# Performance work log

Hardware: AMD Instinct MI355X
Metric: run time of the kernel (lower is better)

Reference implementation:

```python
import jax, jax.numpy as jnp
import numpy as np

B, L, D_MODEL = 2, 4096, 512
HEADS = 8
DH = D_MODEL // HEADS
M = 266  # round(DH * ln(DH)) = round(64 * 4.1589)


def setup_inputs() -> dict:
    key = jax.random.key(0)
    ks = jax.random.split(key, 12)
    s = 0.02
    d = D_MODEL
    return {
        "query": jax.random.normal(ks[0], (B, L, d), jnp.float32),
        "key": jax.random.normal(ks[1], (B, L, d), jnp.float32),
        "value": jax.random.normal(ks[2], (B, L, d), jnp.float32),
        "Wq": jax.random.normal(ks[3], (d, d), jnp.float32) * s,
        "bq": jnp.zeros((d,), jnp.float32),
        "Wk": jax.random.normal(ks[4], (d, d), jnp.float32) * s,
        "bk": jnp.zeros((d,), jnp.float32),
        "Wv": jax.random.normal(ks[5], (d, d), jnp.float32) * s,
        "bv": jnp.zeros((d,), jnp.float32),
        "Wout": jax.random.normal(ks[6], (d, d), jnp.float32) * s,
        "bout": jnp.zeros((d,), jnp.float32),
        "random_features": jax.random.normal(ks[7], (M, DH), jnp.float32),
    }


def reference(query, key, value, Wq, bq, Wk, bk, Wv, bv, Wout, bout, random_features):
    bs, sl, dm = query.shape
    H, Dh = HEADS, dm // HEADS

    def lin(x, W, b):
        return x @ W.T + b

    def to_heads(x):  # [B,L,dm] -> [L,B,H,Dh]  (matches torch [L,B,H,*] layout)
        return x.reshape(bs, sl, H, Dh).transpose(1, 0, 2, 3)

    q = to_heads(lin(query, Wq, bq))
    k = to_heads(lin(key, Wk, bk))
    v = to_heads(lin(value, Wv, bv))

    scale = dm ** 0.25
    q = q / scale
    k = k / scale

    # project onto random features: W_t is random_features^T, [Dh,M]
    pq = jnp.einsum('lbhd,md->lbhm', q, random_features)
    pk = jnp.einsum('lbhd,md->lbhm', k, random_features)
    # exp kernel: exp(h + x) with h = -||x||^2 / 2
    hq = -0.5 * jnp.sum(q * q, axis=-1, keepdims=True)
    hk = -0.5 * jnp.sum(k * k, axis=-1, keepdims=True)
    q_prime = jnp.exp(hq + pq)  # [L,B,H,M]
    k_prime = jnp.exp(hk + pk)  # [L,B,H,M]

    # Causal FAVOR+ numerator/denominator via prefix-sum recurrence (lax.scan over L)
    def step(carry, xs):
        S, z = carry           # S: [B,H,M,Dh], z: [B,H,M]
        qt, kt, vt = xs        # [B,H,M], [B,H,M], [B,H,Dh]
        S = S + kt[..., None] * vt[..., None, :]
        z = z + kt
        num = jnp.einsum('bhmd,bhm->bhd', S, qt)
        den = jnp.einsum('bhm,bhm->bh', qt, z)
        return (S, z), (num, den)

    S0 = jnp.zeros((bs, H, M, Dh), q.dtype)
    z0 = jnp.zeros((bs, H, M), q.dtype)
    _, (num, den) = jax.lax.scan(step, (S0, z0), (q_prime, k_prime, v))

    attn = num / den[..., None]                     # [L,B,H,Dh]
    ctx = attn.transpose(1, 0, 2, 3).reshape(bs, sl, dm)
    return ctx @ Wout.T + bout
```

## Files before the change

kernel.cpp:

```cpp
#include <hip/hip_runtime.h>
#include <hip/hip_bf16.h>

#define L_ 4096
#define MP 272
#define BH16 16

typedef __attribute__((ext_vector_type(8))) __bf16 bf16x8;
typedef __attribute__((ext_vector_type(4))) float f32x4;

__device__ inline __bf16 f2b(float f) {
    unsigned u = __float_as_uint(f);
    unsigned r = (u + 0x7fffu + ((u >> 16) & 1u)) >> 16;
    unsigned short s = (unsigned short)r;
    return *reinterpret_cast<__bf16*>(&s);
}
__device__ inline float b2f(__bf16 b) {
    unsigned short s = *reinterpret_cast<unsigned short*>(&b);
    return __uint_as_float(((unsigned)s) << 16);
}

#define NW 262144
__global__ __launch_bounds__(256) void prep2(
    const float* __restrict__ Wq, const float* __restrict__ Wk, const float* __restrict__ Wv,
    const float* __restrict__ Wout, const float* __restrict__ RF,
    __bf16* __restrict__ Wqb, __bf16* __restrict__ Wkb, __bf16* __restrict__ Wvb,
    __bf16* __restrict__ Woutb, __bf16* __restrict__ RFb, __bf16* __restrict__ vT)
{
    long idx = (long)blockIdx.x * 256 + threadIdx.x;
    if (idx < NW) { Wqb[idx] = f2b(Wq[idx]); return; }  idx -= NW;
    if (idx < NW) { Wkb[idx] = f2b(Wk[idx]); return; }  idx -= NW;
    if (idx < NW) { Wvb[idx] = f2b(Wv[idx]); return; }  idx -= NW;
    if (idx < NW) { Woutb[idx] = f2b(Wout[idx]); return; }  idx -= NW;
    if (idx < MP * 64) { int row = (int)(idx >> 6); RFb[idx] = f2b(row < 266 ? RF[idx] : 0.f); return; }
    idx -= MP * 64;
    if (idx < 65536) {
        int bh = (int)(idx >> 12), l = (int)(idx & 4095);
        vT[((size_t)bh * 65 + 64) * L_ + l] = f2b(1.f);
    }
}

__global__ __launch_bounds__(256) void norms(
    const __bf16* __restrict__ qh, const __bf16* __restrict__ kh,
    float* __restrict__ hq, float* __restrict__ hk)
{
    int idx = blockIdx.x * 256 + threadIdx.x;
    int row = idx >> 2, qq = idx & 3;
    const __bf16* src = row < 65536 ? qh : kh;
    float* dst = row < 65536 ? hq : hk;
    int r = row & 65535;
    const uint4* p = (const uint4*)(src + (size_t)r * 64 + qq * 16);
    float s = 0.f;
    #pragma unroll
    for (int i = 0; i < 2; ++i) {
        uint4 u = p[i];
        unsigned arr[4] = {u.x, u.y, u.z, u.w};
        #pragma unroll
        for (int j = 0; j < 4; ++j) {
            float a = __uint_as_float(arr[j] << 16);
            float b = __uint_as_float(arr[j] & 0xffff0000u);
            s += a * a + b * b;
        }
    }
    s += __shfl_xor(s, 1);
    s += __shfl_xor(s, 2);
    if (qq == 0) dst[r] = -0.5f * s;
}

template<int AF32, int EPI>
__global__ __launch_bounds__(512) void proj(
    const void* __restrict__ Ap, const __bf16* __restrict__ W,
    const float* __restrict__ bias, void* __restrict__ O,
    float scale)
{
    __shared__ __bf16 Al[128 * 40];
    __shared__ __bf16 Bl[64 * 40];
    const int t = threadIdx.x;
    const int w = t >> 6, lane = t & 63;
    const int m0 = blockIdx.x * 128, n0 = blockIdx.y * 64;

    f32x4 acc[4];
    #pragma unroll
    for (int j = 0; j < 4; ++j) acc[j] = f32x4{0.f,0.f,0.f,0.f};

    float4 a_f[2];
    unsigned a_h[4];
    unsigned b_r[2];

    auto LOADT = [&](int ks) {
        const int kk = ks * 32;
        if constexpr (AF32) {
            const float* A = (const float*)Ap;
            #pragma unroll
            for (int it = 0; it < 2; ++it) {
                int u = t + it * 512; int r = u >> 3, q4 = (u & 7) << 2;
                a_f[it] = *(const float4*)&A[(size_t)(m0 + r) * 512 + kk + q4];
            }
        } else {
            const __bf16* A = (const __bf16*)Ap;
            #pragma unroll
            for (int it = 0; it < 4; ++it) {
                int u = t + it * 512; int r = u >> 4, dw = (u & 15) << 1;
                a_h[it] = *(const unsigned*)&A[(size_t)(m0 + r) * 512 + kk + dw];
            }
        }
        #pragma unroll
        for (int it = 0; it < 2; ++it) {
            int u = t + it * 512; int r = u >> 4, dw = (u & 15) << 1;
            b_r[it] = *(const unsigned*)&W[(size_t)(n0 + r) * 512 + kk + dw];
        }
    };
    auto STORET = [&]() {
        if constexpr (AF32) {
            #pragma unroll
            for (int it = 0; it < 2; ++it) {
                int u = t + it * 512; int r = u >> 3, q4 = (u & 7) << 2;
                __bf16* d = &Al[r * 40 + q4];
                d[0] = f2b(a_f[it].x); d[1] = f2b(a_f[it].y);
                d[2] = f2b(a_f[it].z); d[3] = f2b(a_f[it].w);
            }
        } else {
            #pragma unroll
            for (int it = 0; it < 4; ++it) {
                int u = t + it * 512; int r = u >> 4, dw = (u & 15) << 1;
                *(unsigned*)&Al[r * 40 + dw] = a_h[it];
            }
        }
        #pragma unroll
        for (int it = 0; it < 2; ++it) {
            int u = t + it * 512; int r = u >> 4, dw = (u & 15) << 1;
            *(unsigned*)&Bl[r * 40 + dw] = b_r[it];
        }
    };

    LOADT(0);
    for (int ks = 0; ks < 16; ++ks) {
        __syncthreads();
        STORET();
        __syncthreads();
        if (ks < 15) LOADT(ks + 1);
        bf16x8 af = *(const bf16x8*)&Al[(w * 16 + (lane & 15)) * 40 + (lane >> 4) * 8];
        #pragma unroll
        for (int j = 0; j < 4; ++j) {
            bf16x8 bf = *(const bf16x8*)&Bl[(j * 16 + (lane & 15)) * 40 + (lane >> 4) * 8];
            acc[j] = __builtin_amdgcn_mfma_f32_16x16x32_bf16(af, bf, acc[j], 0, 0, 0);
        }
    }

    if constexpr (EPI == 1) {
        __shared__ __bf16 Tv[64 * 136];
        #pragma unroll
        for (int j = 0; j < 4; ++j)
            #pragma unroll
            for (int e = 0; e < 4; ++e) {
                int rl = w * 16 + ((lane >> 4) << 2) + e;
                int cn = n0 + j * 16 + (lane & 15);
                Tv[(cn & 63) * 136 + rl] = f2b(acc[j][e] + bias[cn]);
            }
        __syncthreads();
        __bf16* vT = (__bf16*)O;
        int b = m0 >> 12, l0 = m0 & 4095, h = n0 >> 6;
        #pragma unroll
        for (int it = 0; it < 2; ++it) {
            int v = t + it * 512;
            int d = v >> 4, seg = v & 15;
            *(uint4*)&vT[((size_t)(b * 8 + h) * 65 + d) * L_ + l0 + seg * 8] =
                *(const uint4*)&Tv[d * 136 + seg * 8];
        }
    } else {
        #pragma unroll
        for (int j = 0; j < 4; ++j)
            #pragma unroll
            for (int e = 0; e < 4; ++e) {
                int r = m0 + w * 16 + ((lane >> 4) << 2) + e;
                int cn = n0 + j * 16 + (lane & 15);
                float val = acc[j][e];
                if constexpr (EPI == 0) {
                    float vv = (val + bias[cn]) * scale;
                    int b = r >> 12, l = r & 4095, h = cn >> 6, d = cn & 63;
                    ((__bf16*)O)[(((size_t)(b * 8 + h) * L_ + l) << 6) + d] = f2b(vv);
                } else {
                    ((float*)O)[(size_t)r * 512 + cn] = val + bias[cn];
                }
            }
    }
}

__global__ __launch_bounds__(256) void rfproj2(
    const __bf16* __restrict__ qh, const __bf16* __restrict__ kh,
    const __bf16* __restrict__ RFb,
    const float* __restrict__ hq, const float* __restrict__ hk,
    __bf16* __restrict__ q_p, __bf16* __restrict__ k_nat)
{
    __shared__ __bf16 Al[64 * 40];
    __shared__ __bf16 Bl[MP * 40];
    const int t = threadIdx.x;
    const int w = t >> 6, lane = t & 63;
    const int l0 = blockIdx.x * 64, bh = blockIdx.y;
    const int zq = blockIdx.z;
    const __bf16* X = (zq ? kh : qh) + (size_t)bh * 262144;
    const float* hrow = (zq ? hk : hq) + (size_t)bh * 4096;
    __bf16* O = (zq ? k_nat : q_p) + (size_t)bh * 1114112;

    f32x4 acc[17];
    #pragma unroll
    for (int j = 0; j < 17; ++j) acc[j] = f32x4{0.f,0.f,0.f,0.f};

    unsigned a_r[4], b_r[17];
    auto LOADT = [&](int ks) {
        const int kk = ks * 32;
        #pragma unroll
        for (int it = 0; it < 4; ++it) {
            int u = t + it * 256; int r = u >> 4, dw = (u & 15) << 1;
            a_r[it] = *(const unsigned*)&X[(size_t)(l0 + r) * 64 + kk + dw];
        }
        #pragma unroll
        for (int it = 0; it < 17; ++it) {
            int u = t + it * 256; int r = u >> 4, dw = (u & 15) << 1;
            b_r[it] = *(const unsigned*)&RFb[(size_t)r * 64 + kk + dw];
        }
    };
    LOADT(0);
    for (int ks = 0; ks < 2; ++ks) {
        __syncthreads();
        #pragma unroll
        for (int it = 0; it < 4; ++it) {
            int u = t + it * 256; int r = u >> 4, dw = (u & 15) << 1;
            *(unsigned*)&Al[r * 40 + dw] = a_r[it];
        }
        #pragma unroll
        for (int it = 0; it < 17; ++it) {
            int u = t + it * 256; int r = u >> 4, dw = (u & 15) << 1;
            *(unsigned*)&Bl[r * 40 + dw] = b_r[it];
        }
        __syncthreads();
        if (ks < 1) LOADT(1);
        bf16x8 af = *(const bf16x8*)&Al[(w * 16 + (lane & 15)) * 40 + (lane >> 4) * 8];
        #pragma unroll
        for (int j = 0; j < 17; ++j) {
            bf16x8 bf = *(const bf16x8*)&Bl[(j * 16 + (lane & 15)) * 40 + (lane >> 4) * 8];
            acc[j] = __builtin_amdgcn_mfma_f32_16x16x32_bf16(af, bf, acc[j], 0, 0, 0);
        }
    }
    #pragma unroll
    for (int j = 0; j < 17; ++j)
        #pragma unroll
        for (int e = 0; e < 4; ++e) {
            int rl = w * 16 + ((lane >> 4) << 2) + e;
            int cn = j * 16 + (lane & 15);
            float h = hrow[l0 + rl];
            float v = (cn < 266) ? __expf(h + acc[j][e]) : 0.f;
            O[(size_t)(l0 + rl) * MP + cn] = f2b(v);
        }
}

__global__ __launch_bounds__(256) void chunk_sums3(
    const __bf16* __restrict__ k_nat, const __bf16* __restrict__ vT,
    __bf16* __restrict__ ScT)
{
    __shared__ __bf16 Al[64 * 72];
    __shared__ __bf16 Bl[80 * 72];
    __shared__ __bf16 T2[80 * 72];
    const int t = threadIdx.x;
    const int w = t >> 6, lane = t & 63;
    const int m0 = blockIdx.x * 64;
    const int z = blockIdx.z, zb = z & 15, zc = z >> 4;
    const __bf16* A = k_nat + (size_t)zb * 1114112 + (size_t)(zc * 64) * MP;
    const __bf16* B = vT + (size_t)zb * 266240 + (size_t)zc * 64;

    #pragma unroll
    for (int it = 0; it < 8; ++it) {
        int u = t + it * 256; int l = u >> 5, mp = (u & 31) << 1;
        unsigned v = (m0 + mp < MP) ? *(const unsigned*)&A[(size_t)l * MP + m0 + mp] : 0u;
        unsigned short lo = (unsigned short)(v & 0xffffu), hi = (unsigned short)(v >> 16);
        Al[mp * 72 + l] = *reinterpret_cast<__bf16*>(&lo);
        Al[(mp + 1) * 72 + l] = *reinterpret_cast<__bf16*>(&hi);
    }
    #pragma unroll
    for (int it = 0; it < 10; ++it) {
        int u = t + it * 256; int d = u >> 5, lp = (u & 31) << 1;
        unsigned v = (d < 65) ? *(const unsigned*)&B[(size_t)d * L_ + lp] : 0u;
        *(unsigned*)&Bl[d * 72 + lp] = v;
    }
    __syncthreads();
    f32x4 acc[5];
    #pragma unroll
    for (int j = 0; j < 5; ++j) acc[j] = f32x4{0.f,0.f,0.f,0.f};
    #pragma unroll
    for (int ks = 0; ks < 2; ++ks) {
        const int kk = ks * 32;
        bf16x8 af = *(const bf16x8*)&Al[(w * 16 + (lane & 15)) * 72 + kk + (lane >> 4) * 8];
        #pragma unroll
        for (int j = 0; j < 5; ++j) {
            bf16x8 bf = *(const bf16x8*)&Bl[(j * 16 + (lane & 15)) * 72 + kk + (lane >> 4) * 8];
            acc[j] = __builtin_amdgcn_mfma_f32_16x16x32_bf16(af, bf, acc[j], 0, 0, 0);
        }
    }
    #pragma unroll
    for (int j = 0; j < 5; ++j)
        #pragma unroll
        for (int e = 0; e < 4; ++e) {
            int rl = w * 16 + ((lane >> 4) << 2) + e;
            int cn = j * 16 + (lane & 15);
            T2[cn * 72 + rl] = f2b(acc[j][e]);
        }
    __syncthreads();
    __bf16* Obase = ScT + (size_t)(zc * 16 + zb) * 17680;
    for (int v2 = t; v2 < 65 * 8; v2 += 256) {
        int row = v2 >> 3, seg = v2 & 7;
        if (m0 + seg * 8 < MP)
            *(uint4*)&Obase[(size_t)row * MP + m0 + seg * 8] = *(const uint4*)&T2[row * 72 + seg * 8];
    }
}

__global__ __launch_bounds__(256) void prefixk(__bf16* __restrict__ ScT)
{
    int idx = blockIdx.x * 256 + threadIdx.x;
    const int STRIDE = BH16 * 65 * MP;
    if (idx >= STRIDE) return;
    __bf16* p = ScT + idx;
    float run = 0.f;
    #pragma unroll 1
    for (int cb = 0; cb < 8; ++cb) {
        float v[8];
        #pragma unroll
        for (int i = 0; i < 8; ++i) v[i] = b2f(p[(size_t)(cb * 8 + i) * STRIDE]);
        #pragma unroll
        for (int i = 0; i < 8; ++i) { p[(size_t)(cb * 8 + i) * STRIDE] = f2b(run); run += v[i]; }
    }
}

__global__ __launch_bounds__(256) void fusedD(
    const __bf16* __restrict__ q_p, const __bf16* __restrict__ k_nat,
    const __bf16* __restrict__ ScT, const __bf16* __restrict__ vT,
    __bf16* __restrict__ ctx)
{
    __shared__ __bf16 Aq[64 * 40];
    __shared__ __bf16 B1l[64 * 40];
    __shared__ __bf16 B2l[80 * 40];
    __shared__ __bf16 Vl[80 * 72];
    __shared__ __bf16 Sl[64 * 72];
    __shared__ float sden[64];
    const int t = threadIdx.x;
    const int w = t >> 6, lane = t & 63;
    const int z = blockIdx.x, zb = z & 15, zc = z >> 4;
    const __bf16* qp_b = q_p + (size_t)zb * 1114112 + (size_t)(zc * 64) * MP;
    const __bf16* kn_b = k_nat + (size_t)zb * 1114112 + (size_t)(zc * 64) * MP;
    const __bf16* Sp_b = ScT + (size_t)(zc * 16 + zb) * 17680;
    const __bf16* vT_b = vT + (size_t)zb * 266240 + (size_t)zc * 64;

    unsigned v_r[10];
    #pragma unroll
    for (int it = 0; it < 10; ++it) {
        int u = t + it * 256; int d = u >> 5, lp = (u & 31) << 1;
        v_r[it] = (d < 65) ? *(const unsigned*)&vT_b[(size_t)d * L_ + lp] : 0u;
    }

    unsigned a_r[4], b_r[4], c_r[5];
    auto LOADT = [&](int ks) {
        const int kk = ks * 32;
        #pragma unroll
        for (int it = 0; it < 4; ++it) {
            int u = t + it * 256; int r = u >> 4, dw = (u & 15) << 1;
            bool ok = (kk + dw) < MP;
            a_r[it] = ok ? *(const unsigned*)&qp_b[(size_t)r * MP + kk + dw] : 0u;
            b_r[it] = ok ? *(const unsigned*)&kn_b[(size_t)r * MP + kk + dw] : 0u;
        }
        #pragma unroll
        for (int it = 0; it < 5; ++it) {
            int u = t + it * 256; int r = u >> 4, dw = (u & 15) << 1;
            c_r[it] = (r < 65 && (kk + dw) < MP) ? *(const unsigned*)&Sp_b[(size_t)r * MP + kk + dw] : 0u;
        }
    };

    f32x4 acc1[4], acc2[5];
    #pragma unroll
    for (int j = 0; j < 4; ++j) acc1[j] = f32x4{0.f,0.f,0.f,0.f};
    #pragma unroll
    for (int j = 0; j < 5; ++j) acc2[j] = f32x4{0.f,0.f,0.f,0.f};

    LOADT(0);
    for (int ks = 0; ks < 9; ++ks) {
        __syncthreads();
        #pragma unroll
        for (int it = 0; it < 4; ++it) {
            int u = t + it * 256; int r = u >> 4, dw = (u & 15) << 1;
            *(unsigned*)&Aq[r * 40 + dw] = a_r[it];
            *(unsigned*)&B1l[r * 40 + dw] = b_r[it];
        }
        #pragma unroll
        for (int it = 0; it < 5; ++it) {
            int u = t + it * 256; int r = u >> 4, dw = (u & 15) << 1;
            *(unsigned*)&B2l[r * 40 + dw] = c_r[it];
        }
        __syncthreads();
        if (ks < 8) LOADT(ks + 1);
        bf16x8 af = *(const bf16x8*)&Aq[(w * 16 + (lane & 15)) * 40 + (lane >> 4) * 8];
        #pragma unroll
        for (int j = 0; j < 4; ++j) {
            bf16x8 bf = *(const bf16x8*)&B1l[(j * 16 + (lane & 15)) * 40 + (lane >> 4) * 8];
            acc1[j] = __builtin_amdgcn_mfma_f32_16x16x32_bf16(af, bf, acc1[j], 0, 0, 0);
        }
        #pragma unroll
        for (int j = 0; j < 5; ++j) {
            bf16x8 bf = *(const bf16x8*)&B2l[(j * 16 + (lane & 15)) * 40 + (lane >> 4) * 8];
            acc2[j] = __builtin_amdgcn_mfma_f32_16x16x32_bf16(af, bf, acc2[j], 0, 0, 0);
        }
    }
    #pragma unroll
    for (int it = 0; it < 10; ++it) {
        int u = t + it * 256; int d = u >> 5, lp = (u & 31) << 1;
        *(unsigned*)&Vl[d * 72 + lp] = v_r[it];
    }
    #pragma unroll
    for (int j = 0; j < 4; ++j)
        #pragma unroll
        for (int e = 0; e < 4; ++e) {
            int rl = w * 16 + ((lane >> 4) << 2) + e;
            int cn = j * 16 + (lane & 15);
            Sl[rl * 72 + cn] = f2b(rl >= cn ? acc1[j][e] : 0.f);
        }
    __syncthreads();
    #pragma unroll
    for (int ks2 = 0; ks2 < 2; ++ks2) {
        const int kk = ks2 * 32;
        bf16x8 as = *(const bf16x8*)&Sl[(w * 16 + (lane & 15)) * 72 + kk + (lane >> 4) * 8];
        #pragma unroll
        for (int j = 0; j < 5; ++j) {
            bf16x8 bf = *(const bf16x8*)&Vl[(j * 16 + (lane & 15)) * 72 + kk + (lane >> 4) * 8];
            acc2[j] = __builtin_amdgcn_mfma_f32_16x16x32_bf16(as, bf, acc2[j], 0, 0, 0);
        }
    }
    if ((lane & 15) == 0) {
        #pragma unroll
        for (int e = 0; e < 4; ++e)
            sden[w * 16 + ((lane >> 4) << 2) + e] = acc2[4][e];
    }
    __syncthreads();
    const int b = zb >> 3, h = zb & 7;
    #pragma unroll
    for (int j = 0; j < 4; ++j)
        #pragma unroll
        for (int e = 0; e < 4; ++e) {
            int rl = w * 16 + ((lane >> 4) << 2) + e;
            int cn = j * 16 + (lane & 15);
            float val = acc2[j][e] / sden[rl];
            ctx[((size_t)(b * L_ + zc * 64 + rl)) * 512 + h * 64 + cn] = f2b(val);
        }
}

extern "C" void kernel_launch(void* const* d_in, const int* in_sizes, int n_in,
                              void* d_out, int out_size, void* d_ws, size_t ws_size,
                              hipStream_t stream) {
    const float* query = (const float*)d_in[0];
    const float* key   = (const float*)d_in[1];
    const float* value = (const float*)d_in[2];
    const float* Wq    = (const float*)d_in[3];
    const float* bq    = (const float*)d_in[4];
    const float* Wk    = (const float*)d_in[5];
    const float* bk    = (const float*)d_in[6];
    const float* Wv    = (const float*)d_in[7];
    const float* bv    = (const float*)d_in[8];
    const float* Wout  = (const float*)d_in[9];
    const float* bout  = (const float*)d_in[10];
    const float* RF    = (const float*)d_in[11];

    char* w8 = (char*)d_ws;
    __bf16* ctx  = (__bf16*)(w8 + 0);
    __bf16* qh   = (__bf16*)(w8 + 0);
    __bf16* kh   = (__bf16*)(w8 + 8388608);
    __bf16* vT   = (__bf16*)(w8 + 16777216);
    __bf16* k_nat= (__bf16*)(w8 + 25296896);
    __bf16* ScT  = (__bf16*)(w8 + 60948480);
    __bf16* q_p  = (__bf16*)(w8 + 97157120);
    __bf16* Wqb  = (__bf16*)(w8 + 132808704);
    __bf16* Wkb  = (__bf16*)(w8 + 133332992);
    __bf16* Wvb  = (__bf16*)(w8 + 133857280);
    __bf16* Woutb= (__bf16*)(w8 + 134381568);
    __bf16* RFb  = (__bf16*)(w8 + 134905856);
    float*  hq   = (float*) (w8 + 134940672);
    float*  hk   = (float*) (w8 + 135202816);

    const float qscale = 0.21022410381342865f;

    prep2<<<4420, 256, 0, stream>>>(Wq, Wk, Wv, Wout, RF, Wqb, Wkb, Wvb, Woutb, RFb, vT);

    dim3 gg(64, 8);
    proj<1,0><<<gg, 512, 0, stream>>>(query, Wqb, bq, qh, qscale);
    proj<1,0><<<gg, 512, 0, stream>>>(key,   Wkb, bk, kh, qscale);
    proj<1,1><<<gg, 512, 0, stream>>>(value, Wvb, bv, vT, 1.f);

    norms<<<2048, 256, 0, stream>>>(qh, kh, hq, hk);

    rfproj2<<<dim3(64,16,2), 256, 0, stream>>>(qh, kh, RFb, hq, hk, q_p, k_nat);

    chunk_sums3<<<dim3(5,1,1024), 256, 0, stream>>>(k_nat, vT, ScT);

    prefixk<<<1105, 256, 0, stream>>>(ScT);

    fusedD<<<1024, 256, 0, stream>>>(q_p, k_nat, ScT, vT, ctx);

    proj<0,2><<<gg, 512, 0, stream>>>(ctx, Woutb, bout, d_out, 1.f);
}
```

Baseline: 270.3 us.

## Fuse random-feature projection into chunk-sum and attention kernels, fold norms into projection

Removes the standalone norms and rfproj2 kernels. The squared-norm reduction now runs in the Q/K projection epilogue using warp shuffles. The exp(h + x·RF) feature maps are recomputed on chip inside chunk_sums4 and fusedD2 instead of being written to and re-read from large q_p/k_nat buffers in global memory. This cuts two launches and a lot of HBM traffic, in exchange for recomputing the key features twice and loading RF tiles in a per-m-tile loop with extra synchronisation.

```diff
diff --git a/kernel.cpp b/kernel.cpp
--- a/kernel.cpp
+++ b/kernel.cpp
@@ -39,38 +39,11 @@
     }
 }
 
-__global__ __launch_bounds__(256) void norms(
-    const __bf16* __restrict__ qh, const __bf16* __restrict__ kh,
-    float* __restrict__ hq, float* __restrict__ hk)
-{
-    int idx = blockIdx.x * 256 + threadIdx.x;
-    int row = idx >> 2, qq = idx & 3;
-    const __bf16* src = row < 65536 ? qh : kh;
-    float* dst = row < 65536 ? hq : hk;
-    int r = row & 65535;
-    const uint4* p = (const uint4*)(src + (size_t)r * 64 + qq * 16);
-    float s = 0.f;
-    #pragma unroll
-    for (int i = 0; i < 2; ++i) {
-        uint4 u = p[i];
-        unsigned arr[4] = {u.x, u.y, u.z, u.w};
-        #pragma unroll
-        for (int j = 0; j < 4; ++j) {
-            float a = __uint_as_float(arr[j] << 16);
-            float b = __uint_as_float(arr[j] & 0xffff0000u);
-            s += a * a + b * b;
-        }
-    }
-    s += __shfl_xor(s, 1);
-    s += __shfl_xor(s, 2);
-    if (qq == 0) dst[r] = -0.5f * s;
-}
-
 template<int AF32, int EPI>
 __global__ __launch_bounds__(512) void proj(
     const void* __restrict__ Ap, const __bf16* __restrict__ W,
     const float* __restrict__ bias, void* __restrict__ O,
-    float scale)
+    float* __restrict__ hout, float scale)
 {
     __shared__ __bf16 Al[128 * 40];
     __shared__ __bf16 Bl[64 * 40];
@@ -166,149 +139,133 @@
             *(uint4*)&vT[((size_t)(b * 8 + h) * 65 + d) * L_ + l0 + seg * 8] =
                 *(const uint4*)&Tv[d * 136 + seg * 8];
         }
-    } else {
+    } else if constexpr (EPI == 0) {
+        float sred[4] = {0.f, 0.f, 0.f, 0.f};
         #pragma unroll
         for (int j = 0; j < 4; ++j)
             #pragma unroll
             for (int e = 0; e < 4; ++e) {
                 int r = m0 + w * 16 + ((lane >> 4) << 2) + e;
                 int cn = n0 + j * 16 + (lane & 15);
-                float val = acc[j][e];
-                if constexpr (EPI == 0) {
-                    float vv = (val + bias[cn]) * scale;
-                    int b = r >> 12, l = r & 4095, h = cn >> 6, d = cn & 63;
-                    ((__bf16*)O)[(((size_t)(b * 8 + h) * L_ + l) << 6) + d] = f2b(vv);
-                } else {
-                    ((float*)O)[(size_t)r * 512 + cn] = val + bias[cn];
-                }
-            }
-    }
-}
-
-__global__ __launch_bounds__(256) void rfproj2(
-    const __bf16* __restrict__ qh, const __bf16* __restrict__ kh,
-    const __bf16* __restrict__ RFb,
-    const float* __restrict__ hq, const float* __restrict__ hk,
-    __bf16* __restrict__ q_p, __bf16* __restrict__ k_nat)
+                float vv = (acc[j][e] + bias[cn]) * scale;
+                int b = r >> 12, l = r & 4095, h = cn >> 6, d = cn & 63;
+                ((__bf16*)O)[(((size_t)(b * 8 + h) * L_ + l) << 6) + d] = f2b(vv);
+                sred[e] += vv * vv;
+            }
+        #pragma unroll
+        for (int e = 0; e < 4; ++e) {
+            float s = sred[e];
+            s += __shfl_xor(s, 1); s += __shfl_xor(s, 2);
+            s += __shfl_xor(s, 4); s += __shfl_xor(s, 8);
+            if ((lane & 15) == 0) {
+                int r = m0 + w * 16 + ((lane >> 4) << 2) + e;
+                int bh = (r >> 12) * 8 + (n0 >> 6);
+                hout[(size_t)bh * 4096 + (r & 4095)] = -0.5f * s;
+            }
+        }
+    } else {
+        #pragma unroll
+        for (int j = 0; j < 4; ++j)
+            #pragma unroll
+            for (int e = 0; e < 4; ++e) {
+                int r = m0 + w * 16 + ((lane >> 4) << 2) + e;
+                int cn = n0 + j * 16 + (lane & 15);
+                ((float*)O)[(size_t)r * 512 + cn] = acc[j][e] + bias[cn];
+            }
+    }
+}
+
+__global__ __launch_bounds__(256) void chunk_sums4(
+    const __bf16* __restrict__ kh, const __bf16* __restrict__ vT,
+    const float* __restrict__ hk, const __bf16* __restrict__ RFb,
+    __bf16* __restrict__ ScT)
 {
-    __shared__ __bf16 Al[64 * 40];
-    __shared__ __bf16 Bl[MP * 40];
+    __shared__ char arena[41472];
+    __bf16* RFl = (__bf16*)(arena);
+    __bf16* KPl = (__bf16*)(arena + 9216);
+    __bf16* Vl  = (__bf16*)(arena + 18432);
+    __bf16* T2  = (__bf16*)(arena + 29952);
     const int t = threadIdx.x;
     const int w = t >> 6, lane = t & 63;
-    const int l0 = blockIdx.x * 64, bh = blockIdx.y;
-    const int zq = blockIdx.z;
-    const __bf16* X = (zq ? kh : qh) + (size_t)bh * 262144;
-    const float* hrow = (zq ? hk : hq) + (size_t)bh * 4096;
-    __bf16* O = (zq ? k_nat : q_p) + (size_t)bh * 1114112;
-
-    f32x4 acc[17];
-    #pragma unroll
-    for (int j = 0; j < 17; ++j) acc[j] = f32x4{0.f,0.f,0.f,0.f};
-
-    unsigned a_r[4], b_r[17];
-    auto LOADT = [&](int ks) {
-        const int kk = ks * 32;
-        #pragma unroll
-        for (int it = 0; it < 4; ++it) {
-            int u = t + it * 256; int r = u >> 4, dw = (u & 15) << 1;
-            a_r[it] = *(const unsigned*)&X[(size_t)(l0 + r) * 64 + kk + dw];
-        }
-        #pragma unroll
-        for (int it = 0; it < 17; ++it) {
-            int u = t + it * 256; int r = u >> 4, dw = (u & 15) << 1;
-            b_r[it] = *(const unsigned*)&RFb[(size_t)r * 64 + kk + dw];
-        }
-    };
-    LOADT(0);
-    for (int ks = 0; ks < 2; ++ks) {
-        __syncthreads();
-        #pragma unroll
-        for (int it = 0; it < 4; ++it) {
-            int u = t + it * 256; int r = u >> 4, dw = (u & 15) << 1;
-            *(unsigned*)&Al[r * 40 + dw] = a_r[it];
-        }
-        #pragma unroll
-        for (int it = 0; it < 17; ++it) {
-            int u = t + it * 256; int r = u >> 4, dw = (u & 15) << 1;
-            *(unsigned*)&Bl[r * 40 + dw] = b_r[it];
-        }
-        __syncthreads();
-        if (ks < 1) LOADT(1);
-        bf16x8 af = *(const bf16x8*)&Al[(w * 16 + (lane & 15)) * 40 + (lane >> 4) * 8];
-        #pragma unroll
-        for (int j = 0; j < 17; ++j) {
-            bf16x8 bf = *(const bf16x8*)&Bl[(j * 16 + (lane & 15)) * 40 + (lane >> 4) * 8];
-            acc[j] = __builtin_amdgcn_mfma_f32_16x16x32_bf16(af, bf, acc[j], 0, 0, 0);
-        }
-    }
-    #pragma unroll
-    for (int j = 0; j < 17; ++j)
-        #pragma unroll
-        for (int e = 0; e < 4; ++e) {
-            int rl = w * 16 + ((lane >> 4) << 2) + e;
-            int cn = j * 16 + (lane & 15);
-            float h = hrow[l0 + rl];
-            float v = (cn < 266) ? __expf(h + acc[j][e]) : 0.f;
-            O[(size_t)(l0 + rl) * MP + cn] = f2b(v);
-        }
-}
-
-__global__ __launch_bounds__(256) void chunk_sums3(
-    const __bf16* __restrict__ k_nat, const __bf16* __restrict__ vT,
-    __bf16* __restrict__ ScT)
-{
-    __shared__ __bf16 Al[64 * 72];
-    __shared__ __bf16 Bl[80 * 72];
-    __shared__ __bf16 T2[80 * 72];
-    const int t = threadIdx.x;
-    const int w = t >> 6, lane = t & 63;
-    const int m0 = blockIdx.x * 64;
-    const int z = blockIdx.z, zb = z & 15, zc = z >> 4;
-    const __bf16* A = k_nat + (size_t)zb * 1114112 + (size_t)(zc * 64) * MP;
-    const __bf16* B = vT + (size_t)zb * 266240 + (size_t)zc * 64;
-
-    #pragma unroll
-    for (int it = 0; it < 8; ++it) {
-        int u = t + it * 256; int l = u >> 5, mp = (u & 31) << 1;
-        unsigned v = (m0 + mp < MP) ? *(const unsigned*)&A[(size_t)l * MP + m0 + mp] : 0u;
-        unsigned short lo = (unsigned short)(v & 0xffffu), hi = (unsigned short)(v >> 16);
-        Al[mp * 72 + l] = *reinterpret_cast<__bf16*>(&lo);
-        Al[(mp + 1) * 72 + l] = *reinterpret_cast<__bf16*>(&hi);
-    }
-    #pragma unroll
-    for (int it = 0; it < 10; ++it) {
-        int u = t + it * 256; int d = u >> 5, lp = (u & 31) << 1;
-        unsigned v = (d < 65) ? *(const unsigned*)&B[(size_t)d * L_ + lp] : 0u;
-        *(unsigned*)&Bl[d * 72 + lp] = v;
-    }
-    __syncthreads();
-    f32x4 acc[5];
-    #pragma unroll
-    for (int j = 0; j < 5; ++j) acc[j] = f32x4{0.f,0.f,0.f,0.f};
-    #pragma unroll
-    for (int ks = 0; ks < 2; ++ks) {
-        const int kk = ks * 32;
-        bf16x8 af = *(const bf16x8*)&Al[(w * 16 + (lane & 15)) * 72 + kk + (lane >> 4) * 8];
-        #pragma unroll
-        for (int j = 0; j < 5; ++j) {
-            bf16x8 bf = *(const bf16x8*)&Bl[(j * 16 + (lane & 15)) * 72 + kk + (lane >> 4) * 8];
-            acc[j] = __builtin_amdgcn_mfma_f32_16x16x32_bf16(af, bf, acc[j], 0, 0, 0);
-        }
-    }
-    #pragma unroll
-    for (int j = 0; j < 5; ++j)
-        #pragma unroll
-        for (int e = 0; e < 4; ++e) {
-            int rl = w * 16 + ((lane >> 4) << 2) + e;
-            int cn = j * 16 + (lane & 15);
-            T2[cn * 72 + rl] = f2b(acc[j][e]);
-        }
-    __syncthreads();
+    const int z = blockIdx.x, zb = z & 15, zc = z >> 4;
+    const __bf16* kh_b = kh + (size_t)zb * 262144 + (size_t)(zc * 64) * 64;
+    const __bf16* vT_b = vT + (size_t)zb * 266240 + (size_t)zc * 64;
     __bf16* Obase = ScT + (size_t)(zc * 16 + zb) * 17680;
-    for (int v2 = t; v2 < 65 * 8; v2 += 256) {
-        int row = v2 >> 3, seg = v2 & 7;
-        if (m0 + seg * 8 < MP)
-            *(uint4*)&Obase[(size_t)row * MP + m0 + seg * 8] = *(const uint4*)&T2[row * 72 + seg * 8];
+
+    bf16x8 ak[2];
+    #pragma unroll
+    for (int ks = 0; ks < 2; ++ks)
+        ak[ks] = *(const bf16x8*)&kh_b[(size_t)(w * 16 + (lane & 15)) * 64 + ks * 32 + (lane >> 4) * 8];
+    float hkr[4];
+    #pragma unroll
+    for (int e = 0; e < 4; ++e)
+        hkr[e] = hk[(size_t)zb * 4096 + zc * 64 + w * 16 + ((lane >> 4) << 2) + e];
+
+    #pragma unroll
+    for (int it = 0; it < 9; ++it) {
+        int u = t + it * 256;
+        if (u < 2080) {
+            int d = u >> 5, lp = (u & 31) << 1;
+            *(unsigned*)&Vl[d * 72 + lp] = *(const unsigned*)&vT_b[(size_t)d * L_ + lp];
+        }
+    }
+
+    for (int mt = 0; mt < 5; ++mt) {
+        const int m0 = mt * 64;
+        __syncthreads();
+        #pragma unroll
+        for (int it = 0; it < 8; ++it) {
+            int u = t + it * 256; int r = u >> 5, lp = (u & 31) << 1;
+            unsigned v = (m0 + r < MP) ? *(const unsigned*)&RFb[(size_t)(m0 + r) * 64 + lp] : 0u;
+            *(unsigned*)&RFl[r * 72 + lp] = v;
+        }
+        __syncthreads();
+        f32x4 acck[4];
+        #pragma unroll
+        for (int j = 0; j < 4; ++j) acck[j] = f32x4{0.f,0.f,0.f,0.f};
+        #pragma unroll
+        for (int ks = 0; ks < 2; ++ks)
+            #pragma unroll
+            for (int j = 0; j < 4; ++j) {
+                bf16x8 bf = *(const bf16x8*)&RFl[(j * 16 + (lane & 15)) * 72 + ks * 32 + (lane >> 4) * 8];
+                acck[j] = __builtin_amdgcn_mfma_f32_16x16x32_bf16(ak[ks], bf, acck[j], 0, 0, 0);
+            }
+        #pragma unroll
+        for (int j = 0; j < 4; ++j)
+            #pragma unroll
+            for (int e = 0; e < 4; ++e) {
+                int rl = w * 16 + ((lane >> 4) << 2) + e;
+                int cn = j * 16 + (lane & 15);
+                float v = (m0 + cn < 266) ? __expf(hkr[e] + acck[j][e]) : 0.f;
+                KPl[cn * 72 + rl] = f2b(v);
+            }
+        __syncthreads();
+        f32x4 accS[5];
+        #pragma unroll
+        for (int j = 0; j < 5; ++j) accS[j] = f32x4{0.f,0.f,0.f,0.f};
+        #pragma unroll
+        for (int ks = 0; ks < 2; ++ks) {
+            bf16x8 af = *(const bf16x8*)&KPl[(w * 16 + (lane & 15)) * 72 + ks * 32 + (lane >> 4) * 8];
+            #pragma unroll
+            for (int j = 0; j < 5; ++j) {
+                bf16x8 bf = *(const bf16x8*)&Vl[(j * 16 + (lane & 15)) * 72 + ks * 32 + (lane >> 4) * 8];
+                accS[j] = __builtin_amdgcn_mfma_f32_16x16x32_bf16(af, bf, accS[j], 0, 0, 0);
+            }
+        }
+        #pragma unroll
+        for (int j = 0; j < 5; ++j)
+            #pragma unroll
+            for (int e = 0; e < 4; ++e) {
+                int rl = w * 16 + ((lane >> 4) << 2) + e;
+                int cn = j * 16 + (lane & 15);
+                T2[cn * 72 + rl] = f2b(accS[j][e]);
+            }
+        __syncthreads();
+        for (int v2 = t; v2 < 65 * 8; v2 += 256) {
+            int row = v2 >> 3, seg = v2 & 7;
+            if (m0 + seg * 8 < MP)
+                *(uint4*)&Obase[(size_t)row * MP + m0 + seg * 8] = *(const uint4*)&T2[row * 72 + seg * 8];
+        }
     }
 }
 
@@ -329,25 +286,42 @@
     }
 }
 
-__global__ __launch_bounds__(256) void fusedD(
-    const __bf16* __restrict__ q_p, const __bf16* __restrict__ k_nat,
-    const __bf16* __restrict__ ScT, const __bf16* __restrict__ vT,
-    __bf16* __restrict__ ctx)
+__global__ __launch_bounds__(256) void fusedD2(
+    const __bf16* __restrict__ qh, const __bf16* __restrict__ kh,
+    const float* __restrict__ hq, const float* __restrict__ hk,
+    const __bf16* __restrict__ RFb, const __bf16* __restrict__ ScT,
+    const __bf16* __restrict__ vT, __bf16* __restrict__ ctx)
 {
-    __shared__ __bf16 Aq[64 * 40];
-    __shared__ __bf16 B1l[64 * 40];
-    __shared__ __bf16 B2l[80 * 40];
-    __shared__ __bf16 Vl[80 * 72];
-    __shared__ __bf16 Sl[64 * 72];
-    __shared__ float sden[64];
+    __shared__ char arena[41728];
+    __bf16* RFl = (__bf16*)(arena);
+    __bf16* Vl  = (__bf16*)(arena);
+    __bf16* B2l = (__bf16*)(arena + 11520);
+    __bf16* Aq  = (__bf16*)(arena + 23040);
+    __bf16* Bk  = (__bf16*)(arena + 32256);
+    __bf16* Sl  = (__bf16*)(arena + 32256);
+    float* sden = (float*)(arena + 41472);
     const int t = threadIdx.x;
     const int w = t >> 6, lane = t & 63;
     const int z = blockIdx.x, zb = z & 15, zc = z >> 4;
-    const __bf16* qp_b = q_p + (size_t)zb * 1114112 + (size_t)(zc * 64) * MP;
-    const __bf16* kn_b = k_nat + (size_t)zb * 1114112 + (size_t)(zc * 64) * MP;
+    const __bf16* qh_b = qh + (size_t)zb * 262144 + (size_t)(zc * 64) * 64;
+    const __bf16* kh_b = kh + (size_t)zb * 262144 + (size_t)(zc * 64) * 64;
     const __bf16* Sp_b = ScT + (size_t)(zc * 16 + zb) * 17680;
     const __bf16* vT_b = vT + (size_t)zb * 266240 + (size_t)zc * 64;
 
+    bf16x8 aq[2], ak[2];
+    #pragma unroll
+    for (int ks = 0; ks < 2; ++ks) {
+        size_t off = (size_t)(w * 16 + (lane & 15)) * 64 + ks * 32 + (lane >> 4) * 8;
+        aq[ks] = *(const bf16x8*)&qh_b[off];
+        ak[ks] = *(const bf16x8*)&kh_b[off];
+    }
+    float hqr[4], hkr[4];
+    #pragma unroll
+    for (int e = 0; e < 4; ++e) {
+        int rl = w * 16 + ((lane >> 4) << 2) + e;
+        hqr[e] = hq[(size_t)zb * 4096 + zc * 64 + rl];
+        hkr[e] = hk[(size_t)zb * 4096 + zc * 64 + rl];
+    }
     unsigned v_r[10];
     #pragma unroll
     for (int it = 0; it < 10; ++it) {
@@ -355,57 +329,69 @@
         v_r[it] = (d < 65) ? *(const unsigned*)&vT_b[(size_t)d * L_ + lp] : 0u;
     }
 
-    unsigned a_r[4], b_r[4], c_r[5];
-    auto LOADT = [&](int ks) {
-        const int kk = ks * 32;
-        #pragma unroll
-        for (int it = 0; it < 4; ++it) {
-            int u = t + it * 256; int r = u >> 4, dw = (u & 15) << 1;
-            bool ok = (kk + dw) < MP;
-            a_r[it] = ok ? *(const unsigned*)&qp_b[(size_t)r * MP + kk + dw] : 0u;
-            b_r[it] = ok ? *(const unsigned*)&kn_b[(size_t)r * MP + kk + dw] : 0u;
-        }
-        #pragma unroll
-        for (int it = 0; it < 5; ++it) {
-            int u = t + it * 256; int r = u >> 4, dw = (u & 15) << 1;
-            c_r[it] = (r < 65 && (kk + dw) < MP) ? *(const unsigned*)&Sp_b[(size_t)r * MP + kk + dw] : 0u;
-        }
-    };
-
     f32x4 acc1[4], acc2[5];
     #pragma unroll
     for (int j = 0; j < 4; ++j) acc1[j] = f32x4{0.f,0.f,0.f,0.f};
     #pragma unroll
     for (int j = 0; j < 5; ++j) acc2[j] = f32x4{0.f,0.f,0.f,0.f};
 
-    LOADT(0);
-    for (int ks = 0; ks < 9; ++ks) {
-        __syncthreads();
-        #pragma unroll
-        for (int it = 0; it < 4; ++it) {
-            int u = t + it * 256; int r = u >> 4, dw = (u & 15) << 1;
-            *(unsigned*)&Aq[r * 40 + dw] = a_r[it];
-            *(unsigned*)&B1l[r * 40 + dw] = b_r[it];
-        }
-        #pragma unroll
-        for (int it = 0; it < 5; ++it) {
-            int u = t + it * 256; int r = u >> 4, dw = (u & 15) << 1;
-            *(unsigned*)&B2l[r * 40 + dw] = c_r[it];
-        }
-        __syncthreads();
-        if (ks < 8) LOADT(ks + 1);
-        bf16x8 af = *(const bf16x8*)&Aq[(w * 16 + (lane & 15)) * 40 + (lane >> 4) * 8];
-        #pragma unroll
-        for (int j = 0; j < 4; ++j) {
-            bf16x8 bf = *(const bf16x8*)&B1l[(j * 16 + (lane & 15)) * 40 + (lane >> 4) * 8];
-            acc1[j] = __builtin_amdgcn_mfma_f32_16x16x32_bf16(af, bf, acc1[j], 0, 0, 0);
-        }
-        #pragma unroll
-        for (int j = 0; j < 5; ++j) {
-            bf16x8 bf = *(const bf16x8*)&B2l[(j * 16 + (lane & 15)) * 40 + (lane >> 4) * 8];
-            acc2[j] = __builtin_amdgcn_mfma_f32_16x16x32_bf16(af, bf, acc2[j], 0, 0, 0);
-        }
-    }
+    for (int mt = 0; mt < 5; ++mt) {
+        const int m0 = mt * 64;
+        __syncthreads();
+        #pragma unroll
+        for (int it = 0; it < 8; ++it) {
+            int u = t + it * 256; int r = u >> 5, lp = (u & 31) << 1;
+            unsigned v = (m0 + r < MP) ? *(const unsigned*)&RFb[(size_t)(m0 + r) * 64 + lp] : 0u;
+            *(unsigned*)&RFl[r * 72 + lp] = v;
+        }
+        #pragma unroll
+        for (int it = 0; it < 9; ++it) {
+            int u = t + it * 256;
+            if (u < 2080) {
+                int r = u >> 5, lp = (u & 31) << 1;
+                unsigned v = (m0 + lp < MP) ? *(const unsigned*)&Sp_b[(size_t)r * MP + m0 + lp] : 0u;
+                *(unsigned*)&B2l[r * 72 + lp] = v;
+            }
+        }
+        __syncthreads();
+        f32x4 accq[4], acck[4];
+        #pragma unroll
+        for (int j = 0; j < 4; ++j) { accq[j] = f32x4{0.f,0.f,0.f,0.f}; acck[j] = f32x4{0.f,0.f,0.f,0.f}; }
+        #pragma unroll
+        for (int ks = 0; ks < 2; ++ks)
+            #pragma unroll
+            for (int j = 0; j < 4; ++j) {
+                bf16x8 bf = *(const bf16x8*)&RFl[(j * 16 + (lane & 15)) * 72 + ks * 32 + (lane >> 4) * 8];
+                accq[j] = __builtin_amdgcn_mfma_f32_16x16x32_bf16(aq[ks], bf, accq[j], 0, 0, 0);
+                acck[j] = __builtin_amdgcn_mfma_f32_16x16x32_bf16(ak[ks], bf, acck[j], 0, 0, 0);
+            }
+        #pragma unroll
+        for (int j = 0; j < 4; ++j)
+            #pragma unroll
+            for (int e = 0; e < 4; ++e) {
+                int rl = w * 16 + ((lane >> 4) << 2) + e;
+                int cn = j * 16 + (lane & 15);
+                bool ok = (m0 + cn) < 266;
+                Aq[rl * 72 + cn] = f2b(ok ? __expf(hqr[e] + accq[j][e]) : 0.f);
+                Bk[rl * 72 + cn] = f2b(ok ? __expf(hkr[e] + acck[j][e]) : 0.f);
+            }
+        __syncthreads();
+        #pragma unroll
+        for (int ks = 0; ks < 2; ++ks) {
+            bf16x8 af = *(const bf16x8*)&Aq[(w * 16 + (lane & 15)) * 72 + ks * 32 + (lane >> 4) * 8];
+            #pragma unroll
+            for (int j = 0; j < 4; ++j) {
+                bf16x8 bf = *(const bf16x8*)&Bk[(j * 16 + (lane & 15)) * 72 + ks * 32 + (lane >> 4) * 8];
+                acc1[j] = __builtin_amdgcn_mfma_f32_16x16x32_bf16(af, bf, acc1[j], 0, 0, 0);
+            }
+            #pragma unroll
+            for (int j = 0; j < 5; ++j) {
+                bf16x8 bf = *(const bf16x8*)&B2l[(j * 16 + (lane & 15)) * 72 + ks * 32 + (lane >> 4) * 8];
+                acc2[j] = __builtin_amdgcn_mfma_f32_16x16x32_bf16(af, bf, acc2[j], 0, 0, 0);
+            }
+        }
+    }
+    __syncthreads();
     #pragma unroll
     for (int it = 0; it < 10; ++it) {
         int u = t + it * 256; int d = u >> 5, lp = (u & 31) << 1;
@@ -422,11 +408,10 @@
     __syncthreads();
     #pragma unroll
     for (int ks2 = 0; ks2 < 2; ++ks2) {
-        const int kk = ks2 * 32;
-        bf16x8 as = *(const bf16x8*)&Sl[(w * 16 + (lane & 15)) * 72 + kk + (lane >> 4) * 8];
+        bf16x8 as = *(const bf16x8*)&Sl[(w * 16 + (lane & 15)) * 72 + ks2 * 32 + (lane >> 4) * 8];
         #pragma unroll
         for (int j = 0; j < 5; ++j) {
-            bf16x8 bf = *(const bf16x8*)&Vl[(j * 16 + (lane & 15)) * 72 + kk + (lane >> 4) * 8];
+            bf16x8 bf = *(const bf16x8*)&Vl[(j * 16 + (lane & 15)) * 72 + ks2 * 32 + (lane >> 4) * 8];
             acc2[j] = __builtin_amdgcn_mfma_f32_16x16x32_bf16(as, bf, acc2[j], 0, 0, 0);
         }
     }
@@ -466,38 +451,32 @@
 
     char* w8 = (char*)d_ws;
     __bf16* ctx  = (__bf16*)(w8 + 0);
-    __bf16* qh   = (__bf16*)(w8 + 0);
-    __bf16* kh   = (__bf16*)(w8 + 8388608);
-    __bf16* vT   = (__bf16*)(w8 + 16777216);
-    __bf16* k_nat= (__bf16*)(w8 + 25296896);
-    __bf16* ScT  = (__bf16*)(w8 + 60948480);
-    __bf16* q_p  = (__bf16*)(w8 + 97157120);
-    __bf16* Wqb  = (__bf16*)(w8 + 132808704);
-    __bf16* Wkb  = (__bf16*)(w8 + 133332992);
-    __bf16* Wvb  = (__bf16*)(w8 + 133857280);
-    __bf16* Woutb= (__bf16*)(w8 + 134381568);
-    __bf16* RFb  = (__bf16*)(w8 + 134905856);
-    float*  hq   = (float*) (w8 + 134940672);
-    float*  hk   = (float*) (w8 + 135202816);
+    __bf16* qh   = (__bf16*)(w8 + 8388608);
+    __bf16* kh   = (__bf16*)(w8 + 16777216);
+    __bf16* vT   = (__bf16*)(w8 + 25165824);
+    __bf16* ScT  = (__bf16*)(w8 + 33688576);
+    __bf16* Wqb  = (__bf16*)(w8 + 69897216);
+    __bf16* Wkb  = (__bf16*)(w8 + 70421504);
+    __bf16* Wvb  = (__bf16*)(w8 + 70945792);
+    __bf16* Woutb= (__bf16*)(w8 + 71470080);
+    __bf16* RFb  = (__bf16*)(w8 + 71994368);
+    float*  hq   = (float*) (w8 + 72029184);
+    float*  hk   = (float*) (w8 + 72291328);
 
     const float qscale = 0.21022410381342865f;
 
     prep2<<<4420, 256, 0, stream>>>(Wq, Wk, Wv, Wout, RF, Wqb, Wkb, Wvb, Woutb, RFb, vT);
 
     dim3 gg(64, 8);
-    proj<1,0><<<gg, 512, 0, stream>>>(query, Wqb, bq, qh, qscale);
-    proj<1,0><<<gg, 512, 0, stream>>>(key,   Wkb, bk, kh, qscale);
-    proj<1,1><<<gg, 512, 0, stream>>>(value, Wvb, bv, vT, 1.f);
-
-    norms<<<2048, 256, 0, stream>>>(qh, kh, hq, hk);
-
-    rfproj2<<<dim3(64,16,2), 256, 0, stream>>>(qh, kh, RFb, hq, hk, q_p, k_nat);
-
-    chunk_sums3<<<dim3(5,1,1024), 256, 0, stream>>>(k_nat, vT, ScT);
+    proj<1,0><<<gg, 512, 0, stream>>>(query, Wqb, bq, qh, hq, qscale);
+    proj<1,0><<<gg, 512, 0, stream>>>(key,   Wkb, bk, kh, hk, qscale);
+    proj<1,1><<<gg, 512, 0, stream>>>(value, Wvb, bv, vT, nullptr, 1.f);
+
+    chunk_sums4<<<1024, 256, 0, stream>>>(kh, vT, hk, RFb, ScT);
 
     prefixk<<<1105, 256, 0, stream>>>(ScT);
 
-    fusedD<<<1024, 256, 0, stream>>>(q_p, k_nat, ScT, vT, ctx);
-
-    proj<0,2><<<gg, 512, 0, stream>>>(ctx, Woutb, bout, d_out, 1.f);
-}
+    fusedD2<<<1024, 256, 0, stream>>>(qh, kh, hq, hk, RFb, ScT, vT, ctx);
+
+    proj<0,2><<<gg, 512, 0, stream>>>(ctx, Woutb, bout, d_out, nullptr, 1.f);
+}
```

Result: slower. 276.2 us (+2.2%).
